# Kernel optimization log

Hardware: AMD Instinct MI355X
Metric: run time of the kernel (lower is better)

Reference implementation:

```python
import jax, jax.numpy as jnp
import numpy as np

N_NODES = 50000
LN_EPS = 1e-5


def setup_inputs() -> dict:
    key = jax.random.key(0)
    ks = jax.random.split(key, 8)
    d = 128
    E = 800000
    x = jax.random.normal(ks[0], (N_NODES, d), dtype=jnp.float32)
    edge_index = jax.random.randint(ks[1], (2, E), 0, N_NODES, dtype=jnp.int64)
    edge_weight = jax.random.uniform(ks[2], (E,), dtype=jnp.float32)
    s = 1.0 / np.sqrt(d)
    W1 = jax.random.normal(ks[3], (d, d), dtype=jnp.float32) * s
    W2 = jax.random.normal(ks[4], (d, d), dtype=jnp.float32) * s
    return {
        'x': x, 'edge_index': edge_index, 'edge_weight': edge_weight,
        'W1': W1, 'b1': jnp.zeros((d,), jnp.float32),
        'W2': W2, 'b2': jnp.zeros((d,), jnp.float32),
        'g1': jnp.ones((d,), jnp.float32), 'be1': jnp.zeros((d,), jnp.float32),
        'g2': jnp.ones((d,), jnp.float32), 'be2': jnp.zeros((d,), jnp.float32),
    }


def _layer_norm(h, gamma, beta):
    mu = jnp.mean(h, axis=-1, keepdims=True)
    var = jnp.mean(jnp.square(h - mu), axis=-1, keepdims=True)
    return (h - mu) * jax.lax.rsqrt(var + LN_EPS) * gamma + beta


def _gcn_layer(h, W, b, src, dst, ew):
    # GCNConv(add_self_loops=False, normalize=False): linear then edge scatter-add
    h = h @ W                                    # [N, d]
    msg = h[src] * ew[:, None]                   # [E, d] gather + weight
    agg = jax.ops.segment_sum(msg, dst, num_segments=N_NODES)  # scatter-add at target
    return agg + b


def reference(x, edge_index, edge_weight, W1, b1, W2, b2, g1, be1, g2, be2):
    src, dst = edge_index[0], edge_index[1]  # PyG: messages flow source -> target
    h = _gcn_layer(x, W1, b1, src, dst, edge_weight)
    h = jax.nn.relu(_layer_norm(h, g1, be1))  # dropout = identity (eval)
    h = _gcn_layer(h, W2, b2, src, dst, edge_weight)
    h = jax.nn.relu(_layer_norm(h, g2, be2))
    return h
```

## Files before the change

kernel.cpp:

```cpp
#include <hip/hip_runtime.h>
#include <hip/hip_fp16.h>
#include <stdint.h>

#define LN_EPS 1e-5f
#define G1 256
#define P1CAP 4096
#define P3CAP 6144
#define CAPB 6144

typedef __attribute__((ext_vector_type(8))) short s16x8;
typedef __attribute__((ext_vector_type(4))) float f32x4;

__device__ __forceinline__ float b2f(unsigned short u) {
    union { unsigned int i; float f; } v; v.i = ((unsigned int)u) << 16; return v.f;
}
__device__ __forceinline__ unsigned short f2b(float f) {
    union { float f; unsigned int i; } v; v.f = f;
    unsigned int u = v.i;
    return (unsigned short)((u + 0x7fffu + ((u >> 16) & 1u)) >> 16);
}
__device__ __forceinline__ unsigned int pk2(float a, float b) {
    return (unsigned int)f2b(a) | ((unsigned int)f2b(b) << 16);
}
__device__ __forceinline__ __half2 u2h2(unsigned int u) {
    union { unsigned int i; __half2 h; } v; v.i = u; return v.h;
}

__device__ __forceinline__ float rdf(const void* p, int i, int f32flag) {
    return f32flag ? ((const float*)p)[i] : b2f(((const unsigned short*)p)[i]);
}

__global__ __launch_bounds__(256) void k_p1(const unsigned short* __restrict__ xu,
                                            const int* __restrict__ ei, const void* __restrict__ ew,
                                            const void* W1, const void* W2,
                                            const void* b1, const void* b2_,
                                            const void* g1, const void* g2,
                                            const void* be1, const void* be2,
                                            unsigned short* __restrict__ Wt1,
                                            unsigned short* __restrict__ Wt2,
                                            float* __restrict__ sm,
                                            int E, int B, int chunk,
                                            unsigned int* __restrict__ gA,
                                            unsigned char* __restrict__ g8,
                                            int* __restrict__ cnt2d, int* __restrict__ lofs2d,
                                            int* __restrict__ flags) {
    __shared__ int hist[256], cur[256], tmp[256];
    __shared__ unsigned int bin32[P1CAP];
    __shared__ unsigned char bin8[P1CAP];
    int t = threadIdx.x, g = blockIdx.x;
    if (t < 2) hist[t] = 0;
    __syncthreads();
    int c1 = 0;
    for (int i = t; i < 2048; i += 256)
        if (fabsf(b2f(xu[i])) > 1e6f) ++c1;
    if (c1) atomicAdd(&hist[0], c1);
    int mn = (E < 1024) ? E : 1024;
    int z = 0;
    for (int i = t; i < mn; i += 256)
        if (ei[2 * i + 1] == 0) ++z;
    if (z) atomicAdd(&hist[1], z);
    __syncthreads();
    int f32f = (hist[0] > 32) ? 1 : 0;
    int f64  = (hist[1] > (mn >> 1)) ? 1 : 0;
    if (g == 0 && t == 0) { flags[0] = f32f; flags[1] = f64; }

    if (g >= G1) {
        int i = (g - G1) * 256 + t;
        int k = i >> 7, j = i & 127;
        Wt1[j * 128 + k] = f2b(rdf(W1, i, f32f));
        Wt2[j * 128 + k] = f2b(rdf(W2, i, f32f));
        if (g == G1 && t < 128) {
            sm[t]       = rdf(b1, t, f32f);
            sm[128 + t] = rdf(b2_, t, f32f);
            sm[256 + t] = rdf(g1, t, f32f);
            sm[384 + t] = rdf(g2, t, f32f);
            sm[512 + t] = rdf(be1, t, f32f);
            sm[640 + t] = rdf(be2, t, f32f);
        }
        return;
    }
    __syncthreads();
    int base = g * chunk;
    int cnt = E - base; if (cnt > chunk) cnt = chunk; if (cnt < 0) cnt = 0;
    hist[t] = 0;
    __syncthreads();
    for (int i = t; i < cnt; i += 256) {
        int e = base + i;
        int d = f64 ? ei[2 * E + 2 * e] : ei[E + e];
        atomicAdd(&hist[d >> 8], 1);
    }
    __syncthreads();
    int v = hist[t];
    tmp[t] = v;
    __syncthreads();
    for (int d = 1; d < 256; d <<= 1) {
        int x = (t >= d) ? tmp[t - d] : 0;
        __syncthreads();
        tmp[t] += x;
        __syncthreads();
    }
    int excl = tmp[t] - v;
    cur[t] = excl;
    if (t < B) { cnt2d[t * G1 + g] = v; lofs2d[t * G1 + g] = excl; }
    __syncthreads();
    for (int i = t; i < cnt; i += 256) {
        int e = base + i;
        int d, sN;
        if (f64) { d = ei[2 * E + 2 * e]; sN = ei[2 * e]; }
        else     { d = ei[E + e];         sN = ei[e]; }
        float w = f32f ? ((const float*)ew)[e] : b2f(((const unsigned short*)ew)[e]);
        __half wh = __float2half(w);
        int p = atomicAdd(&cur[d >> 8], 1);
        bin32[p] = (unsigned int)(sN & 0xffff) | ((unsigned int)__half_as_ushort(wh) << 16);
        bin8[p]  = (unsigned char)(d & 255);
    }
    __syncthreads();
    for (int j = t; j < cnt; j += 256) {
        gA[base + j] = bin32[j];
        g8[base + j] = bin8[j];
    }
}

__global__ __launch_bounds__(256) void k_p3g(const unsigned int* __restrict__ gA,
                                             const unsigned char* __restrict__ g8,
                                             const int* __restrict__ cnt2d,
                                             const int* __restrict__ lofs2d,
                                             unsigned int* __restrict__ edata,
                                             uint2* __restrict__ nfo,
                                             const void* __restrict__ X,
                                             const unsigned short* __restrict__ Wt,
                                             unsigned short* __restrict__ Hh,
                                             const int* __restrict__ flags,
                                             int N, int B, int chunk) {
    __shared__ unsigned char lds[49152];
    int t = threadIdx.x, g = blockIdx.x;

    if (g < B) {
        unsigned int* raw = (unsigned int*)lds;
        unsigned char* r8 = lds + 24576;
        int* h   = (int*)(lds + 30720);
        int* tmp = (int*)(lds + 31744);
        int* s_cnt = (int*)(lds + 32768);
        int b = g;
        int segc = cnt2d[b * G1 + t];
        int sbase = t * chunk + lofs2d[b * G1 + t];
        int v = segc;
        tmp[t] = v;
        __syncthreads();
        for (int d = 1; d < 256; d <<= 1) {
            int x = (t >= d) ? tmp[t - d] : 0;
            __syncthreads();
            tmp[t] += x;
            __syncthreads();
        }
        int lo = tmp[t] - v;
        if (t == 255) s_cnt[0] = tmp[255];
        int j = 0;
        for (; j + 3 < segc; j += 4) {
            unsigned int a0 = gA[sbase + j], a1 = gA[sbase + j + 1];
            unsigned int a2 = gA[sbase + j + 2], a3 = gA[sbase + j + 3];
            unsigned char c0 = g8[sbase + j], c1 = g8[sbase + j + 1];
            unsigned char c2 = g8[sbase + j + 2], c3 = g8[sbase + j + 3];
            int i0 = lo + j;
            if (i0 + 3 < P3CAP) {
                raw[i0] = a0; raw[i0 + 1] = a1; raw[i0 + 2] = a2; raw[i0 + 3] = a3;
                r8[i0] = c0; r8[i0 + 1] = c1; r8[i0 + 2] = c2; r8[i0 + 3] = c3;
            }
        }
        for (; j < segc; ++j) {
            int idx = lo + j;
            if (idx < P3CAP) { raw[idx] = gA[sbase + j]; r8[idx] = g8[sbase + j]; }
        }
        h[t] = 0;
        __syncthreads();
        int cnt = s_cnt[0]; if (cnt > P3CAP) cnt = P3CAP;
        for (int i = t; i < cnt; i += 256) atomicAdd(&h[r8[i]], 1);
        __syncthreads();
        int deg = h[t];
        int pd = (deg + 7) & ~7;
        tmp[t] = pd;
        __syncthreads();
        for (int d = 1; d < 256; d <<= 1) {
            int x = (t >= d) ? tmp[t - d] : 0;
            __syncthreads();
            tmp[t] += x;
            __syncthreads();
        }
        int pexcl = tmp[t] - pd;
        int padTot = tmp[255]; if (padTot > CAPB) padTot = CAPB;
        int node0 = b << 8;
        int gbase = b * CAPB;
        if (node0 + t < N) nfo[node0 + t] = make_uint2((unsigned)(gbase + pexcl), (unsigned)deg);
        h[t] = pexcl;
        for (int i = t; i < padTot; i += 256) edata[gbase + i] = 0;
        __syncthreads();
        for (int i = t; i < cnt; i += 256) {
            int p = atomicAdd(&h[r8[i]], 1);
            if (p < CAPB) edata[gbase + p] = raw[i];
        }
        return;
    }

    unsigned char* xs = lds;
    unsigned char* wt = lds + 16384;
    int node0 = (g - B) * 64;
    int f32in = flags[0];

#pragma unroll
    for (int it = 0; it < 8; ++it) {
        int c = t + it * 256;
        int row = c >> 4, cc = c & 15;
        uint4 v = *(const uint4*)(Wt + row * 128 + cc * 8);
        int off = (row * 256 + cc * 16) ^ ((row & 7) << 4);
        *(uint4*)(wt + off) = v;
    }
#pragma unroll
    for (int it = 0; it < 4; ++it) {
        int c = t + it * 256;
        int row = c >> 4, cc = c & 15;
        int gg = node0 + row;
        uint4 v = make_uint4(0, 0, 0, 0);
        if (gg < N) {
            if (f32in) {
                const float* xr = (const float*)X + (size_t)gg * 128 + cc * 8;
                float4 f0 = *(const float4*)xr;
                float4 f1 = *(const float4*)(xr + 4);
                v.x = pk2(f0.x, f0.y); v.y = pk2(f0.z, f0.w);
                v.z = pk2(f1.x, f1.y); v.w = pk2(f1.z, f1.w);
            } else {
                v = *(const uint4*)((const unsigned short*)X + (size_t)gg * 128 + cc * 8);
            }
        }
        int off = (row * 256 + cc * 16) ^ ((row & 7) << 4);
        *(uint4*)(xs + off) = v;
    }
    __syncthreads();

    int w = t >> 6, l = t & 63;
    int arow = l & 15;
    int apart = l >> 4;
    f32x4 acc[8];
#pragma unroll
    for (int ct = 0; ct < 8; ++ct) acc[ct] = (f32x4){0.f, 0.f, 0.f, 0.f};

#pragma unroll
    for (int ks = 0; ks < 4; ++ks) {
        int grow = w * 16 + arow;
        int aoff = (grow * 256 + ks * 64 + apart * 16) ^ ((grow & 7) << 4);
        s16x8 afrag = *(const s16x8*)(xs + aoff);
#pragma unroll
        for (int ct = 0; ct < 8; ++ct) {
            int brow = ct * 16 + arow;
            int boff = (brow * 256 + ks * 64 + apart * 16) ^ ((brow & 7) << 4);
            s16x8 bfrag = *(const s16x8*)(wt + boff);
            acc[ct] = __builtin_amdgcn_mfma_f32_16x16x32_bf16(afrag, bfrag, acc[ct], 0, 0, 0);
        }
    }
    int orow0 = node0 + w * 16 + apart * 4;
    int ocol = arow;
#pragma unroll
    for (int ct = 0; ct < 8; ++ct) {
#pragma unroll
        for (int r = 0; r < 4; ++r) {
            int gg = orow0 + r;
            if (gg < N) {
                __half hh = __float2half(acc[ct][r]);
                Hh[(size_t)gg * 128 + ct * 16 + ocol] = __half_as_ushort(hh);
            }
        }
    }
}

__global__ __launch_bounds__(256) void k_gemm(const unsigned short* __restrict__ X,
                                              const unsigned short* __restrict__ Wt,
                                              unsigned short* __restrict__ Hh, int N) {
    __shared__ unsigned char lds[49152];
    unsigned char* xs = lds;
    unsigned char* wt = lds + 16384;
    int t = threadIdx.x;
    int node0 = blockIdx.x * 64;

#pragma unroll
    for (int it = 0; it < 8; ++it) {
        int c = t + it * 256;
        int row = c >> 4, cc = c & 15;
        uint4 v = *(const uint4*)(Wt + row * 128 + cc * 8);
        int off = (row * 256 + cc * 16) ^ ((row & 7) << 4);
        *(uint4*)(wt + off) = v;
    }
#pragma unroll
    for (int it = 0; it < 4; ++it) {
        int c = t + it * 256;
        int row = c >> 4, cc = c & 15;
        int g = node0 + row;
        uint4 v = make_uint4(0, 0, 0, 0);
        if (g < N) v = *(const uint4*)(X + (size_t)g * 128 + cc * 8);
        int off = (row * 256 + cc * 16) ^ ((row & 7) << 4);
        *(uint4*)(xs + off) = v;
    }
    __syncthreads();

    int w = t >> 6, l = t & 63;
    int arow = l & 15;
    int apart = l >> 4;
    f32x4 acc[8];
#pragma unroll
    for (int ct = 0; ct < 8; ++ct) acc[ct] = (f32x4){0.f, 0.f, 0.f, 0.f};

#pragma unroll
    for (int ks = 0; ks < 4; ++ks) {
        int grow = w * 16 + arow;
        int aoff = (grow * 256 + ks * 64 + apart * 16) ^ ((grow & 7) << 4);
        s16x8 afrag = *(const s16x8*)(xs + aoff);
#pragma unroll
        for (int ct = 0; ct < 8; ++ct) {
            int brow = ct * 16 + arow;
            int boff = (brow * 256 + ks * 64 + apart * 16) ^ ((brow & 7) << 4);
            s16x8 bfrag = *(const s16x8*)(wt + boff);
            acc[ct] = __builtin_amdgcn_mfma_f32_16x16x32_bf16(afrag, bfrag, acc[ct], 0, 0, 0);
        }
    }
    int orow0 = node0 + w * 16 + apart * 4;
    int ocol = arow;
#pragma unroll
    for (int ct = 0; ct < 8; ++ct) {
#pragma unroll
        for (int r = 0; r < 4; ++r) {
            int g = orow0 + r;
            if (g < N) {
                __half hh = __float2half(acc[ct][r]);
                Hh[(size_t)g * 128 + ct * 16 + ocol] = __half_as_ushort(hh);
            }
        }
    }
}

template <bool FINAL>
__global__ __launch_bounds__(256) void k_agg_ln(const unsigned short* __restrict__ Hh,
                                                const unsigned int* __restrict__ edata,
                                                const uint2* __restrict__ nfo,
                                                const float* __restrict__ bias,
                                                const float* __restrict__ g,
                                                const float* __restrict__ be,
                                                unsigned short* __restrict__ outb,
                                                void* __restrict__ outAny,
                                                const int* __restrict__ flags, int N) {
    int t = threadIdx.x;
    int l16 = t & 15;
    int node = blockIdx.x * 16 + (t >> 4);
    if (node >= N) return;
    uint2 info = nfo[node];
    int base = (int)info.x, deg = (int)info.y;
    __half2 a01 = u2h2(0u), a23 = u2h2(0u), a45 = u2h2(0u), a67 = u2h2(0u);
    const uint4* Hl = (const uint4*)Hh + l16;
    for (int b0 = 0; b0 < deg; b0 += 8) {
        const uint4* ep = (const uint4*)(edata + base + b0);
        uint4 q0 = ep[0], q1 = ep[1];
        uint4 h0 = Hl[(size_t)(q0.x & 0xffffu) << 4];
        uint4 h1 = Hl[(size_t)(q0.y & 0xffffu) << 4];
        uint4 h2 = Hl[(size_t)(q0.z & 0xffffu) << 4];
        uint4 h3 = Hl[(size_t)(q0.w & 0xffffu) << 4];
        uint4 h4 = Hl[(size_t)(q1.x & 0xffffu) << 4];
        uint4 h5 = Hl[(size_t)(q1.y & 0xffffu) << 4];
        uint4 h6 = Hl[(size_t)(q1.z & 0xffffu) << 4];
        uint4 h7 = Hl[(size_t)(q1.w & 0xffffu) << 4];
        unsigned int wb; __half2 w2;
#define ACC8(hh, wsrc)                                                        \
        wb = (wsrc) >> 16; w2 = u2h2(wb | (wb << 16));                        \
        a01 = __hfma2(u2h2(hh.x), w2, a01); a23 = __hfma2(u2h2(hh.y), w2, a23); \
        a45 = __hfma2(u2h2(hh.z), w2, a45); a67 = __hfma2(u2h2(hh.w), w2, a67);
        ACC8(h0, q0.x) ACC8(h1, q0.y) ACC8(h2, q0.z) ACC8(h3, q0.w)
        ACC8(h4, q1.x) ACC8(h5, q1.y) ACC8(h6, q1.z) ACC8(h7, q1.w)
#undef ACC8
    }
    float4 bv0 = ((const float4*)bias)[2 * l16];
    float4 bv1 = ((const float4*)bias)[2 * l16 + 1];
    float a0 = __low2float(a01) + bv0.x, a1 = __high2float(a01) + bv0.y;
    float a2 = __low2float(a23) + bv0.z, a3 = __high2float(a23) + bv0.w;
    float a4 = __low2float(a45) + bv1.x, a5 = __high2float(a45) + bv1.y;
    float a6 = __low2float(a67) + bv1.z, a7 = __high2float(a67) + bv1.w;
    float s = ((a0 + a1) + (a2 + a3)) + ((a4 + a5) + (a6 + a7));
#pragma unroll
    for (int m = 8; m >= 1; m >>= 1) s += __shfl_xor(s, m, 64);
    float mu = s * (1.f / 128.f);
    float d0 = a0 - mu, d1 = a1 - mu, d2 = a2 - mu, d3 = a3 - mu;
    float d4 = a4 - mu, d5 = a5 - mu, d6 = a6 - mu, d7 = a7 - mu;
    float q = ((d0 * d0 + d1 * d1) + (d2 * d2 + d3 * d3)) +
              ((d4 * d4 + d5 * d5) + (d6 * d6 + d7 * d7));
#pragma unroll
    for (int m = 8; m >= 1; m >>= 1) q += __shfl_xor(q, m, 64);
    float rs = rsqrtf(q * (1.f / 128.f) + LN_EPS);
    float4 gv0 = ((const float4*)g)[2 * l16], gv1 = ((const float4*)g)[2 * l16 + 1];
    float4 bev0 = ((const float4*)be)[2 * l16], bev1 = ((const float4*)be)[2 * l16 + 1];
    float r0 = fmaxf(d0 * rs * gv0.x + bev0.x, 0.f);
    float r1 = fmaxf(d1 * rs * gv0.y + bev0.y, 0.f);
    float r2 = fmaxf(d2 * rs * gv0.z + bev0.z, 0.f);
    float r3 = fmaxf(d3 * rs * gv0.w + bev0.w, 0.f);
    float r4 = fmaxf(d4 * rs * gv1.x + bev1.x, 0.f);
    float r5 = fmaxf(d5 * rs * gv1.y + bev1.y, 0.f);
    float r6 = fmaxf(d6 * rs * gv1.z + bev1.z, 0.f);
    float r7 = fmaxf(d7 * rs * gv1.w + bev1.w, 0.f);
    if (FINAL) {
        if (flags[0]) {
            float4* o = (float4*)outAny + (size_t)node * 32 + 2 * l16;
            o[0] = make_float4(r0, r1, r2, r3);
            o[1] = make_float4(r4, r5, r6, r7);
        } else {
            uint4 o;
            o.x = pk2(r0, r1); o.y = pk2(r2, r3);
            o.z = pk2(r4, r5); o.w = pk2(r6, r7);
            ((uint4*)outAny)[(size_t)node * 16 + l16] = o;
        }
    } else {
        uint4 o;
        o.x = pk2(r0, r1); o.y = pk2(r2, r3);
        o.z = pk2(r4, r5); o.w = pk2(r6, r7);
        ((uint4*)outb)[(size_t)node * 16 + l16] = o;
    }
}

extern "C" void kernel_launch(void* const* d_in, const int* in_sizes, int n_in,
                              void* d_out, int out_size, void* d_ws, size_t ws_size,
                              hipStream_t stream) {
    const unsigned short* x_u16 = (const unsigned short*)d_in[0];
    const int*            ei    = (const int*)d_in[1];

    const int N = in_sizes[0] / 128;
    const int E = in_sizes[2];
    const int B = (N + 255) >> 8;
    const int chunk = (E + G1 - 1) / G1;

    unsigned short* Xb = (unsigned short*)d_ws;
    unsigned short* Hh = Xb + (size_t)N * 128;
    unsigned int* gA    = (unsigned int*)(Hh + (size_t)N * 128);
    unsigned int* edata = gA + E;
    unsigned char* g8   = (unsigned char*)(edata + (size_t)B * CAPB);
    int* cnt2d  = (int*)(g8 + ((E + 3) & ~3));
    int* lofs2d = cnt2d + 65536;
    uint2* nfo  = (uint2*)(lofs2d + 65536);
    int* flags  = (int*)(nfo + N);
    unsigned short* Wt1 = (unsigned short*)(flags + 8);
    unsigned short* Wt2 = Wt1 + 16384;
    float* sm   = (float*)(Wt2 + 16384);
    float* b1f  = sm;
    float* b2f_ = sm + 128;
    float* g1f  = sm + 256;
    float* g2f  = sm + 384;
    float* be1f = sm + 512;
    float* be2f = sm + 640;

    const int nodeBlocks = (N + 15) / 16;
    const int gemmBlocks = (N + 63) / 64;

    k_p1<<<G1 + 64, 256, 0, stream>>>(x_u16, ei, d_in[2],
                                      d_in[3], d_in[5], d_in[4], d_in[6],
                                      d_in[7], d_in[9], d_in[8], d_in[10],
                                      Wt1, Wt2, sm,
                                      E, B, chunk, gA, g8, cnt2d, lofs2d, flags);

    k_p3g<<<B + gemmBlocks, 256, 0, stream>>>(gA, g8, cnt2d, lofs2d, edata, nfo,
                                              d_in[0], Wt1, Hh, flags, N, B, chunk);

    k_agg_ln<false><<<nodeBlocks, 256, 0, stream>>>(Hh, edata, nfo, b1f, g1f, be1f, Xb, nullptr, flags, N);

    k_gemm<<<gemmBlocks, 256, 0, stream>>>(Xb, Wt2, Hh, N);
    k_agg_ln<true><<<nodeBlocks, 256, 0, stream>>>(Hh, edata, nfo, b2f_, g2f, be2f, nullptr, d_out, flags, N);
}
```

Before: 110.0 us.

## Fuse layer-1 aggregation+LayerNorm with layer-2 GEMM into one kernel

Replaces the separate layer-1 aggregate/LayerNorm kernel and the layer-2 GEMM kernel with one fused kernel. Each 16-node block aggregates neighbours, applies LayerNorm and ReLU, stages the bf16 result in LDS, then runs MFMA against W2 to write the layer-2 features directly. This removes one launch and the global round trip of the intermediate activations. In exchange, each 16-row block reloads the full 32KB W2 tile into LDS, and the MFMA work per block shrinks, so there is more redundant weight traffic and smaller GEMM tiles.

```diff
diff --git a/kernel.cpp b/kernel.cpp
--- a/kernel.cpp
+++ b/kernel.cpp
@@ -271,78 +271,132 @@
     }
 }
 
-__global__ __launch_bounds__(256) void k_gemm(const unsigned short* __restrict__ X,
-                                              const unsigned short* __restrict__ Wt,
-                                              unsigned short* __restrict__ Hh, int N) {
-    __shared__ unsigned char lds[49152];
-    unsigned char* xs = lds;
-    unsigned char* wt = lds + 16384;
+__global__ __launch_bounds__(256) void k_agg_gemm(const unsigned short* __restrict__ Hh,
+                                                  const unsigned int* __restrict__ edata,
+                                                  const uint2* __restrict__ nfo,
+                                                  const float* __restrict__ bias,
+                                                  const float* __restrict__ g,
+                                                  const float* __restrict__ be,
+                                                  const unsigned short* __restrict__ W2t,
+                                                  unsigned short* __restrict__ Hh2,
+                                                  int N) {
+    __shared__ unsigned char lds[36864];
+    unsigned char* wt = lds;
+    unsigned char* xs = lds + 32768;
     int t = threadIdx.x;
-    int node0 = blockIdx.x * 64;
-
+    int node0 = blockIdx.x * 16;
 #pragma unroll
     for (int it = 0; it < 8; ++it) {
         int c = t + it * 256;
         int row = c >> 4, cc = c & 15;
-        uint4 v = *(const uint4*)(Wt + row * 128 + cc * 8);
+        uint4 v = *(const uint4*)(W2t + row * 128 + cc * 8);
         int off = (row * 256 + cc * 16) ^ ((row & 7) << 4);
         *(uint4*)(wt + off) = v;
     }
-#pragma unroll
-    for (int it = 0; it < 4; ++it) {
-        int c = t + it * 256;
-        int row = c >> 4, cc = c & 15;
-        int g = node0 + row;
-        uint4 v = make_uint4(0, 0, 0, 0);
-        if (g < N) v = *(const uint4*)(X + (size_t)g * 128 + cc * 8);
-        int off = (row * 256 + cc * 16) ^ ((row & 7) << 4);
-        *(uint4*)(xs + off) = v;
-    }
-    __syncthreads();
-
+    int l16 = t & 15;
+    int nodeLocal = t >> 4;
+    int node = node0 + nodeLocal;
+    uint4 xv = make_uint4(0, 0, 0, 0);
+    if (node < N) {
+        uint2 info = nfo[node];
+        int base = (int)info.x, deg = (int)info.y;
+        __half2 a01 = u2h2(0u), a23 = u2h2(0u), a45 = u2h2(0u), a67 = u2h2(0u);
+        const uint4* Hl = (const uint4*)Hh + l16;
+        for (int b0 = 0; b0 < deg; b0 += 8) {
+            const uint4* ep = (const uint4*)(edata + base + b0);
+            uint4 q0 = ep[0], q1 = ep[1];
+            uint4 h0 = Hl[(size_t)(q0.x & 0xffffu) << 4];
+            uint4 h1 = Hl[(size_t)(q0.y & 0xffffu) << 4];
+            uint4 h2 = Hl[(size_t)(q0.z & 0xffffu) << 4];
+            uint4 h3 = Hl[(size_t)(q0.w & 0xffffu) << 4];
+            uint4 h4 = Hl[(size_t)(q1.x & 0xffffu) << 4];
+            uint4 h5 = Hl[(size_t)(q1.y & 0xffffu) << 4];
+            uint4 h6 = Hl[(size_t)(q1.z & 0xffffu) << 4];
+            uint4 h7 = Hl[(size_t)(q1.w & 0xffffu) << 4];
+            unsigned int wb; __half2 w2;
+#define ACC8(hh, wsrc)                                                        \
+            wb = (wsrc) >> 16; w2 = u2h2(wb | (wb << 16));                    \
+            a01 = __hfma2(u2h2(hh.x), w2, a01); a23 = __hfma2(u2h2(hh.y), w2, a23); \
+            a45 = __hfma2(u2h2(hh.z), w2, a45); a67 = __hfma2(u2h2(hh.w), w2, a67);
+            ACC8(h0, q0.x) ACC8(h1, q0.y) ACC8(h2, q0.z) ACC8(h3, q0.w)
+            ACC8(h4, q1.x) ACC8(h5, q1.y) ACC8(h6, q1.z) ACC8(h7, q1.w)
+#undef ACC8
+        }
+        float4 bv0 = ((const float4*)bias)[2 * l16];
+        float4 bv1 = ((const float4*)bias)[2 * l16 + 1];
+        float a0 = __low2float(a01) + bv0.x, a1 = __high2float(a01) + bv0.y;
+        float a2 = __low2float(a23) + bv0.z, a3 = __high2float(a23) + bv0.w;
+        float a4 = __low2float(a45) + bv1.x, a5 = __high2float(a45) + bv1.y;
+        float a6 = __low2float(a67) + bv1.z, a7 = __high2float(a67) + bv1.w;
+        float s = ((a0 + a1) + (a2 + a3)) + ((a4 + a5) + (a6 + a7));
+#pragma unroll
+        for (int m = 8; m >= 1; m >>= 1) s += __shfl_xor(s, m, 64);
+        float mu = s * (1.f / 128.f);
+        float d0 = a0 - mu, d1 = a1 - mu, d2 = a2 - mu, d3 = a3 - mu;
+        float d4 = a4 - mu, d5 = a5 - mu, d6 = a6 - mu, d7 = a7 - mu;
+        float q = ((d0 * d0 + d1 * d1) + (d2 * d2 + d3 * d3)) +
+                  ((d4 * d4 + d5 * d5) + (d6 * d6 + d7 * d7));
+#pragma unroll
+        for (int m = 8; m >= 1; m >>= 1) q += __shfl_xor(q, m, 64);
+        float rs = rsqrtf(q * (1.f / 128.f) + LN_EPS);
+        float4 gv0 = ((const float4*)g)[2 * l16], gv1 = ((const float4*)g)[2 * l16 + 1];
+        float4 bev0 = ((const float4*)be)[2 * l16], bev1 = ((const float4*)be)[2 * l16 + 1];
+        float r0 = fmaxf(d0 * rs * gv0.x + bev0.x, 0.f);
+        float r1 = fmaxf(d1 * rs * gv0.y + bev0.y, 0.f);
+        float r2 = fmaxf(d2 * rs * gv0.z + bev0.z, 0.f);
+        float r3 = fmaxf(d3 * rs * gv0.w + bev0.w, 0.f);
+        float r4 = fmaxf(d4 * rs * gv1.x + bev1.x, 0.f);
+        float r5 = fmaxf(d5 * rs * gv1.y + bev1.y, 0.f);
+        float r6 = fmaxf(d6 * rs * gv1.z + bev1.z, 0.f);
+        float r7 = fmaxf(d7 * rs * gv1.w + bev1.w, 0.f);
+        xv.x = pk2(r0, r1); xv.y = pk2(r2, r3);
+        xv.z = pk2(r4, r5); xv.w = pk2(r6, r7);
+    }
+    {
+        int off = (nodeLocal * 256 + l16 * 16) ^ ((nodeLocal & 7) << 4);
+        *(uint4*)(xs + off) = xv;
+    }
+    __syncthreads();
     int w = t >> 6, l = t & 63;
     int arow = l & 15;
     int apart = l >> 4;
-    f32x4 acc[8];
-#pragma unroll
-    for (int ct = 0; ct < 8; ++ct) acc[ct] = (f32x4){0.f, 0.f, 0.f, 0.f};
-
+    f32x4 acc[2];
+    acc[0] = (f32x4){0.f, 0.f, 0.f, 0.f};
+    acc[1] = (f32x4){0.f, 0.f, 0.f, 0.f};
 #pragma unroll
     for (int ks = 0; ks < 4; ++ks) {
-        int grow = w * 16 + arow;
-        int aoff = (grow * 256 + ks * 64 + apart * 16) ^ ((grow & 7) << 4);
+        int aoff = (arow * 256 + ks * 64 + apart * 16) ^ ((arow & 7) << 4);
         s16x8 afrag = *(const s16x8*)(xs + aoff);
 #pragma unroll
-        for (int ct = 0; ct < 8; ++ct) {
+        for (int ct2 = 0; ct2 < 2; ++ct2) {
+            int ct = w * 2 + ct2;
             int brow = ct * 16 + arow;
             int boff = (brow * 256 + ks * 64 + apart * 16) ^ ((brow & 7) << 4);
             s16x8 bfrag = *(const s16x8*)(wt + boff);
-            acc[ct] = __builtin_amdgcn_mfma_f32_16x16x32_bf16(afrag, bfrag, acc[ct], 0, 0, 0);
-        }
-    }
-    int orow0 = node0 + w * 16 + apart * 4;
-    int ocol = arow;
-#pragma unroll
-    for (int ct = 0; ct < 8; ++ct) {
+            acc[ct2] = __builtin_amdgcn_mfma_f32_16x16x32_bf16(afrag, bfrag, acc[ct2], 0, 0, 0);
+        }
+    }
+    int orow0 = node0 + apart * 4;
+#pragma unroll
+    for (int ct2 = 0; ct2 < 2; ++ct2) {
+        int ocol = (w * 2 + ct2) * 16 + arow;
 #pragma unroll
         for (int r = 0; r < 4; ++r) {
-            int g = orow0 + r;
-            if (g < N) {
-                __half hh = __float2half(acc[ct][r]);
-                Hh[(size_t)g * 128 + ct * 16 + ocol] = __half_as_ushort(hh);
+            int gg = orow0 + r;
+            if (gg < N) {
+                __half hh = __float2half(acc[ct2][r]);
+                Hh2[(size_t)gg * 128 + ocol] = __half_as_ushort(hh);
             }
         }
     }
 }
 
-template <bool FINAL>
 __global__ __launch_bounds__(256) void k_agg_ln(const unsigned short* __restrict__ Hh,
                                                 const unsigned int* __restrict__ edata,
                                                 const uint2* __restrict__ nfo,
                                                 const float* __restrict__ bias,
                                                 const float* __restrict__ g,
                                                 const float* __restrict__ be,
-                                                unsigned short* __restrict__ outb,
                                                 void* __restrict__ outAny,
                                                 const int* __restrict__ flags, int N) {
     int t = threadIdx.x;
@@ -400,22 +454,15 @@
     float r5 = fmaxf(d5 * rs * gv1.y + bev1.y, 0.f);
     float r6 = fmaxf(d6 * rs * gv1.z + bev1.z, 0.f);
     float r7 = fmaxf(d7 * rs * gv1.w + bev1.w, 0.f);
-    if (FINAL) {
-        if (flags[0]) {
-            float4* o = (float4*)outAny + (size_t)node * 32 + 2 * l16;
-            o[0] = make_float4(r0, r1, r2, r3);
-            o[1] = make_float4(r4, r5, r6, r7);
-        } else {
-            uint4 o;
-            o.x = pk2(r0, r1); o.y = pk2(r2, r3);
-            o.z = pk2(r4, r5); o.w = pk2(r6, r7);
-            ((uint4*)outAny)[(size_t)node * 16 + l16] = o;
-        }
+    if (flags[0]) {
+        float4* o = (float4*)outAny + (size_t)node * 32 + 2 * l16;
+        o[0] = make_float4(r0, r1, r2, r3);
+        o[1] = make_float4(r4, r5, r6, r7);
     } else {
         uint4 o;
         o.x = pk2(r0, r1); o.y = pk2(r2, r3);
         o.z = pk2(r4, r5); o.w = pk2(r6, r7);
-        ((uint4*)outb)[(size_t)node * 16 + l16] = o;
+        ((uint4*)outAny)[(size_t)node * 16 + l16] = o;
     }
 }
 
@@ -430,8 +477,8 @@
     const int B = (N + 255) >> 8;
     const int chunk = (E + G1 - 1) / G1;
 
-    unsigned short* Xb = (unsigned short*)d_ws;
-    unsigned short* Hh = Xb + (size_t)N * 128;
+    unsigned short* Hh2 = (unsigned short*)d_ws;
+    unsigned short* Hh  = Hh2 + (size_t)N * 128;
     unsigned int* gA    = (unsigned int*)(Hh + (size_t)N * 128);
     unsigned int* edata = gA + E;
     unsigned char* g8   = (unsigned char*)(edata + (size_t)B * CAPB);
@@ -461,8 +508,9 @@
     k_p3g<<<B + gemmBlocks, 256, 0, stream>>>(gA, g8, cnt2d, lofs2d, edata, nfo,
                                               d_in[0], Wt1, Hh, flags, N, B, chunk);
 
-    k_agg_ln<false><<<nodeBlocks, 256, 0, stream>>>(Hh, edata, nfo, b1f, g1f, be1f, Xb, nullptr, flags, N);
-
-    k_gemm<<<gemmBlocks, 256, 0, stream>>>(Xb, Wt2, Hh, N);
-    k_agg_ln<true><<<nodeBlocks, 256, 0, stream>>>(Hh, edata, nfo, b2f_, g2f, be2f, nullptr, d_out, flags, N);
-}
+    k_agg_gemm<<<nodeBlocks, 256, 0, stream>>>(Hh, edata, nfo, b1f, g1f, be1f,
+                                               Wt2, Hh2, N);
+
+    k_agg_ln<<<nodeBlocks, 256, 0, stream>>>(Hh2, edata, nfo, b2f_, g2f, be2f,
+                                             d_out, flags, N);
+}
```

After: 99.89 us. 1.1x faster.
